# Kernel optimization log

Hardware: AMD Instinct MI355X
Metric: run time of the kernel (lower is better)

The kernel has to match this reference:

```python
import jax, jax.numpy as jnp
import numpy as np

WINDOW = (4, 8, 8)  # (T, Wh, Ww)
NUM_HEADS = 4


def _rel_position_index(ws):
    T, Wh, Ww = ws
    coords = np.stack(np.meshgrid(np.arange(T), np.arange(Wh), np.arange(Ww), indexing='ij'))
    cf = coords.reshape(3, -1)  # [3, N]
    rc = (cf[:, :, None] - cf[:, None, :]).transpose(1, 2, 0).astype(np.int64)  # [N, N, 3]
    rc[..., 0] += T - 1
    rc[..., 1] += Wh - 1
    rc[..., 2] += Ww - 1
    rc[..., 0] *= (2 * Wh - 1) * (2 * Ww - 1)
    rc[..., 1] *= (2 * Ww - 1)
    return rc.sum(-1).astype(np.int32)  # [N, N]


def setup_inputs() -> dict:
    key = jax.random.key(0)
    ks = jax.random.split(key, 5)
    B_, C = 1024, 128
    N = WINDOW[0] * WINDOW[1] * WINDOW[2]
    table_len = (2 * WINDOW[0] - 1) * (2 * WINDOW[1] - 1) * (2 * WINDOW[2] - 1)
    return {
        'x': jax.random.normal(ks[0], (B_, N, C), dtype=jnp.float32),
        'q_w': jax.random.normal(ks[1], (C, C), dtype=jnp.float32) * 0.02,
        'kv_w': jax.random.normal(ks[2], (C, 2 * C), dtype=jnp.float32) * 0.02,
        'proj_w': jax.random.normal(ks[3], (C, C), dtype=jnp.float32) * 0.02,
        'proj_b': jnp.zeros((C,), dtype=jnp.float32),
        'rpb_table': jax.random.normal(ks[4], (table_len, NUM_HEADS), dtype=jnp.float32) * 0.02,
        'rel_index': jnp.asarray(_rel_position_index(WINDOW)),
    }


def reference(x, q_w, kv_w, proj_w, proj_b, rpb_table, rel_index):
    B, N, C = x.shape
    H = NUM_HEADS
    Dh = C // H
    T = WINDOW[0]
    interval = WINDOW[1] * WINDOW[2]
    scale = Dh ** -0.5
    # qkv projections (no bias, eval-mode: dropout is identity)
    q = (x @ q_w).reshape(B, N, H, Dh).transpose(0, 2, 1, 3)      # [B,H,N,Dh]
    kv = (x @ kv_w).reshape(B, N, 2, H, Dh)
    k = kv[:, :, 0].transpose(0, 2, 1, 3)                          # [B,H,N,Dh]
    v = kv[:, :, 1].transpose(0, 2, 1, 3)
    all_ids = np.arange(N)
    outs = []
    for i in range(T):  # fixed small loop over time slices
        qb, qe = i * interval, (i + 1) * interval
        other = np.concatenate([all_ids[:qb], all_ids[qe:]])      # keys = all other frames
        q_i = q[:, :, qb:qe]                                      # [B,H,Nq,Dh]
        k_o = k[:, :, other]                                      # [B,H,Nk,Dh]
        v_o = v[:, :, other]
        # gathered relative position bias: [Nq,Nk,H] -> [1,H,Nq,Nk]
        bias = rpb_table[rel_index[qb:qe][:, other]]
        attn = jnp.einsum('bhqd,bhkd->bhqk', q_i * scale, k_o) + bias.transpose(2, 0, 1)[None]
        attn = jax.nn.softmax(attn, axis=-1)
        out = jnp.einsum('bhqk,bhkd->bhqd', attn, v_o)            # [B,H,Nq,Dh]
        outs.append(out.transpose(0, 2, 1, 3).reshape(B, interval, C))
    x_out = jnp.concatenate(outs, axis=1)                         # [B,N,C]
    return x_out @ proj_w + proj_b
```

## Files before the change

kernel.cpp:

```cpp
#include <hip/hip_runtime.h>
#include <hip/hip_bf16.h>


typedef float  f32x16 __attribute__((ext_vector_type(16)));
typedef float  f32x4_ __attribute__((ext_vector_type(4)));
typedef __bf16 bf16x8 __attribute__((ext_vector_type(8)));
typedef __bf16 bf16x2 __attribute__((ext_vector_type(2)));
typedef unsigned int  uint32x4_ __attribute__((ext_vector_type(4)));
typedef unsigned int  uint32x2_ __attribute__((ext_vector_type(2)));

#define MFMA32(a, b, c) __builtin_amdgcn_mfma_f32_32x32x16_bf16((a), (b), (c), 0, 0, 0)

static __device__ __forceinline__ unsigned int packbf2(float a, float b) {
  bf16x2 t = { (__bf16)a, (__bf16)b };
  return __builtin_bit_cast(unsigned int, t);
}
static __device__ __forceinline__ void plswap(unsigned int &a, unsigned int &b) {
  asm volatile("v_permlane32_swap_b32 %0, %1" : "+v"(a), "+v"(b));
}

#define XS_OFF 0
#define QL_OFF 65536
#define KL_OFF 81920
#define VT_OFF 98304
#define OH_OFF 114688

static __device__ __forceinline__ int swzA(int row, int off) {
  return (row << 6) + (off ^ (((row >> 1) & 3) << 4));
}
static __device__ __forceinline__ int swzX(int row, int off) {
  return (row << 8) + (off ^ ((row & 7) << 4));
}
static __device__ __forceinline__ int swzV(int row, int off) {
  return (row << 9) + (off ^ ((row & 7) << 4));
}

__global__ void prep_kernel(const float* __restrict__ qw, const float* __restrict__ kvw,
                            const float* __restrict__ pw, const float* __restrict__ rpb,
                            const int* __restrict__ relidx,
                            float* __restrict__ biasT, unsigned short* __restrict__ qwt,
                            unsigned short* __restrict__ kwt, unsigned short* __restrict__ vwt,
                            unsigned short* __restrict__ pwt) {
  int gid = blockIdx.x * 256 + threadIdx.x;
  if (gid < 262144) {
    int key = gid & 255;
    int ql  = (gid >> 8) & 63;
    int h   = (gid >> 14) & 3;
    int i   = gid >> 16;
    float v;
    if ((key >> 6) == i) v = -1.0e30f;
    else                 v = rpb[relidx[(i * 64 + ql) * 256 + key] * 4 + h];
    biasT[gid] = v;
  } else {
    int wid = gid - 262144;
    if (wid < 16384) {
      int cin = wid & 127, cout = wid >> 7;
      qwt[wid] = __builtin_bit_cast(unsigned short, (__bf16)(qw[cin * 128 + cout] * 0.17677669529663687f));
      kwt[wid] = __builtin_bit_cast(unsigned short, (__bf16)(kvw[cin * 256 + cout]));
      vwt[wid] = __builtin_bit_cast(unsigned short, (__bf16)(kvw[cin * 256 + 128 + cout]));
      pwt[wid] = __builtin_bit_cast(unsigned short, (__bf16)(pw[cin * 128 + cout]));
    }
  }
}

__global__ __launch_bounds__(512, 2) void fused_attn(
    const float* __restrict__ x, const float* __restrict__ biasT,
    const unsigned short* __restrict__ qwt, const unsigned short* __restrict__ kwt,
    const unsigned short* __restrict__ vwt, const unsigned short* __restrict__ pwt,
    const float* __restrict__ proj_b, float* __restrict__ out) {
  __shared__ __align__(16) char smem[131072];
  const int tid  = threadIdx.x;
  const int w    = tid >> 6;
  const int lane = tid & 63;
  const int lq   = lane & 31;
  const int lh   = lane >> 5;
  const int b    = blockIdx.x;

  const float* xb = x + (size_t)b * (256 * 128);
  #pragma unroll
  for (int it = 0; it < 16; ++it) {
    int idx = it * 512 + tid;
    f32x4_ v = ((const f32x4_*)xb)[idx];
    int n = idx >> 5, c4 = idx & 31;
    uint32x2_ wv = { packbf2(v[0], v[1]), packbf2(v[2], v[3]) };
    *(uint32x2_*)(smem + XS_OFF + swzX(n, c4 * 8)) = wv;
  }
  __syncthreads();

  f32x16 yacc[4];
  #pragma unroll
  for (int nt = 0; nt < 4; ++nt)
    #pragma unroll
    for (int r = 0; r < 16; ++r) yacc[nt][r] = 0.0f;

  for (int h = 0; h < 4; ++h) {
    f32x16 qa, ka, va;
    #pragma unroll
    for (int r = 0; r < 16; ++r) { qa[r] = 0.0f; ka[r] = 0.0f; va[r] = 0.0f; }
    const int wrow = h * 32 + lq;
    #pragma unroll
    for (int ks = 0; ks < 8; ++ks) {
      bf16x8 xf = *(const bf16x8*)(smem + XS_OFF + swzX(w * 32 + lq, ks * 32 + lh * 16));
      bf16x8 wq = *(const bf16x8*)(qwt + wrow * 128 + ks * 16 + lh * 8);
      bf16x8 wk = *(const bf16x8*)(kwt + wrow * 128 + ks * 16 + lh * 8);
      bf16x8 wv = *(const bf16x8*)(vwt + wrow * 128 + ks * 16 + lh * 8);
      qa = MFMA32(wq, xf, qa);
      ka = MFMA32(wk, xf, ka);
      va = MFMA32(xf, wv, va);
    }
    #pragma unroll
    for (int g = 0; g < 4; ++g) {
      uint32x2_ q2 = { packbf2(qa[4*g+0], qa[4*g+1]), packbf2(qa[4*g+2], qa[4*g+3]) };
      *(uint32x2_*)(smem + QL_OFF + swzA(w * 32 + lq, g * 16 + lh * 8)) = q2;
      uint32x2_ k2 = { packbf2(ka[4*g+0], ka[4*g+1]), packbf2(ka[4*g+2], ka[4*g+3]) };
      *(uint32x2_*)(smem + KL_OFF + swzA(w * 32 + lq, g * 16 + lh * 8)) = k2;
      uint32x2_ v2 = { packbf2(va[4*g+0], va[4*g+1]), packbf2(va[4*g+2], va[4*g+3]) };
      *(uint32x2_*)(smem + VT_OFF + swzV(lq, w * 64 + g * 16 + lh * 8)) = v2;
    }
    __syncthreads();

    const int iblk   = w >> 1;
    const int qlocal = (w & 1) * 32 + lq;
    const float* biasW = biasT + (((iblk * 4 + h) * 64 + qlocal) * 256);
    bf16x8 qb0 = *(const bf16x8*)(smem + QL_OFF + swzA(w * 32 + lq, lh * 16));
    bf16x8 qb1 = *(const bf16x8*)(smem + QL_OFF + swzA(w * 32 + lq, 32 + lh * 16));

    f32x16 S[8];
    #pragma unroll
    for (int kt = 0; kt < 8; ++kt) {
      f32x16 c;
      #pragma unroll
      for (int g = 0; g < 4; ++g) {
        f32x4_ bv = *(const f32x4_*)(biasW + kt * 32 + lh * 4 + g * 8);
        c[4*g+0] = bv[0]; c[4*g+1] = bv[1]; c[4*g+2] = bv[2]; c[4*g+3] = bv[3];
      }
      bf16x8 ka0 = *(const bf16x8*)(smem + KL_OFF + swzA(kt * 32 + lq, lh * 16));
      bf16x8 ka1 = *(const bf16x8*)(smem + KL_OFF + swzA(kt * 32 + lq, 32 + lh * 16));
      c = MFMA32(ka0, qb0, c);
      c = MFMA32(ka1, qb1, c);
      S[kt] = c;
    }
    float m = -3.0e38f;
    #pragma unroll
    for (int kt = 0; kt < 8; ++kt)
      #pragma unroll
      for (int r = 0; r < 16; ++r) m = fmaxf(m, S[kt][r]);
    m = fmaxf(m, __shfl_xor(m, 32, 64));
    float l = 0.0f;
    #pragma unroll
    for (int kt = 0; kt < 8; ++kt)
      #pragma unroll
      for (int r = 0; r < 16; ++r) { float e = __expf(S[kt][r] - m); S[kt][r] = e; l += e; }
    l += __shfl_xor(l, 32, 64);
    float linv = 1.0f / l;

    f32x16 pv;
    #pragma unroll
    for (int r = 0; r < 16; ++r) pv[r] = 0.0f;
    #pragma unroll
    for (int kt = 0; kt < 8; ++kt) {
      unsigned int pk0 = packbf2(S[kt][0],  S[kt][1]);
      unsigned int pk1 = packbf2(S[kt][2],  S[kt][3]);
      unsigned int pk2 = packbf2(S[kt][4],  S[kt][5]);
      unsigned int pk3 = packbf2(S[kt][6],  S[kt][7]);
      unsigned int pk4 = packbf2(S[kt][8],  S[kt][9]);
      unsigned int pk5 = packbf2(S[kt][10], S[kt][11]);
      unsigned int pk6 = packbf2(S[kt][12], S[kt][13]);
      unsigned int pk7 = packbf2(S[kt][14], S[kt][15]);
      plswap(pk0, pk2); plswap(pk1, pk3);
      plswap(pk4, pk6); plswap(pk5, pk7);
      uint32x4_ f0 = { pk0, pk1, pk2, pk3 };
      uint32x4_ f1 = { pk4, pk5, pk6, pk7 };
      bf16x8 b0 = __builtin_bit_cast(bf16x8, f0);
      bf16x8 b1 = __builtin_bit_cast(bf16x8, f1);
      bf16x8 va0 = *(const bf16x8*)(smem + VT_OFF + swzV(lq, kt * 64 + lh * 16));
      bf16x8 va1 = *(const bf16x8*)(smem + VT_OFF + swzV(lq, kt * 64 + 32 + lh * 16));
      pv = MFMA32(va0, b0, pv);
      pv = MFMA32(va1, b1, pv);
    }
    #pragma unroll
    for (int g = 0; g < 4; ++g) {
      uint32x2_ o2 = { packbf2(pv[4*g+0] * linv, pv[4*g+1] * linv),
                       packbf2(pv[4*g+2] * linv, pv[4*g+3] * linv) };
      *(uint32x2_*)(smem + OH_OFF + swzA(w * 32 + lq, g * 16 + lh * 8)) = o2;
    }
    __syncthreads();

    bf16x8 a0 = *(const bf16x8*)(smem + OH_OFF + swzA(w * 32 + lq, lh * 16));
    bf16x8 a1 = *(const bf16x8*)(smem + OH_OFF + swzA(w * 32 + lq, 32 + lh * 16));
    #pragma unroll
    for (int nt = 0; nt < 4; ++nt) {
      bf16x8 pb0 = *(const bf16x8*)(pwt + (nt * 32 + lq) * 128 + h * 32 + lh * 8);
      bf16x8 pb1 = *(const bf16x8*)(pwt + (nt * 32 + lq) * 128 + h * 32 + 16 + lh * 8);
      yacc[nt] = MFMA32(a0, pb0, yacc[nt]);
      yacc[nt] = MFMA32(a1, pb1, yacc[nt]);
    }
  }

  float* yb = out + (size_t)b * (256 * 128);
  #pragma unroll
  for (int nt = 0; nt < 4; ++nt) {
    float pbv = proj_b[nt * 32 + lq];
    #pragma unroll
    for (int g = 0; g < 4; ++g)
      #pragma unroll
      for (int r2 = 0; r2 < 4; ++r2) {
        int n = w * 32 + 8 * g + 4 * lh + r2;
        yb[n * 128 + nt * 32 + lq] = yacc[nt][4 * g + r2] + pbv;
      }
  }
}

extern "C" void kernel_launch(void* const* d_in, const int* in_sizes, int n_in,
                              void* d_out, int out_size, void* d_ws, size_t ws_size,
                              hipStream_t stream) {
  (void)in_sizes; (void)n_in; (void)out_size; (void)ws_size;
  const float* x      = (const float*)d_in[0];
  const float* qw     = (const float*)d_in[1];
  const float* kvw    = (const float*)d_in[2];
  const float* pw     = (const float*)d_in[3];
  const float* pb     = (const float*)d_in[4];
  const float* rpb    = (const float*)d_in[5];
  const int*   relidx = (const int*)d_in[6];
  float* out = (float*)d_out;

  char* ws = (char*)d_ws;
  float* biasT          = (float*)ws;
  unsigned short* qwt   = (unsigned short*)(ws + 1048576);
  unsigned short* kwt   = (unsigned short*)(ws + 1048576 + 32768);
  unsigned short* vwt   = (unsigned short*)(ws + 1048576 + 65536);
  unsigned short* pwt   = (unsigned short*)(ws + 1048576 + 98304);

  prep_kernel<<<dim3(1088), dim3(256), 0, stream>>>(qw, kvw, pw, rpb, relidx,
                                                    biasT, qwt, kwt, vwt, pwt);
  fused_attn<<<dim3(1024), dim3(512), 0, stream>>>(x, biasT, qwt, kwt, vwt, pwt, pb, out);
}
```

Before: 519.1 us.

## Software-pipeline next-head QKV projection with PV matmul using double-buffered K/V

The per-head loop now computes the next head's Q/K/V projection MFMAs interleaved with the current head's PV MFMAs, writing K/V into double-buffered LDS slots so one barrier per head suffices. Q is kept in registers via permlane swaps instead of going through LDS. The x fragments are hoisted into registers, and the output projection is deferred to a single pass after all heads by writing per-head outputs over the x tile. Softmax max and sum reductions are also restructured into trees. This raises register pressure, which risks spills or lower occupancy.

After: 551.5 us. 6.2% more time.

```diff
diff --git a/kernel.cpp b/kernel.cpp
--- a/kernel.cpp
+++ b/kernel.cpp
@@ -19,11 +19,26 @@
   asm volatile("v_permlane32_swap_b32 %0, %1" : "+v"(a), "+v"(b));
 }
 
-#define XS_OFF 0
-#define QL_OFF 65536
-#define KL_OFF 81920
-#define VT_OFF 98304
-#define OH_OFF 114688
+static __device__ __forceinline__ float max16(const f32x16& v) {
+  float a0 = fmaxf(v[0], v[1]),  a1 = fmaxf(v[2], v[3]);
+  float a2 = fmaxf(v[4], v[5]),  a3 = fmaxf(v[6], v[7]);
+  float a4 = fmaxf(v[8], v[9]),  a5 = fmaxf(v[10], v[11]);
+  float a6 = fmaxf(v[12], v[13]), a7 = fmaxf(v[14], v[15]);
+  float b0 = fmaxf(a0, a1), b1 = fmaxf(a2, a3), b2 = fmaxf(a4, a5), b3 = fmaxf(a6, a7);
+  return fmaxf(fmaxf(b0, b1), fmaxf(b2, b3));
+}
+static __device__ __forceinline__ float sum16(const f32x16& v) {
+  float a0 = v[0] + v[1],  a1 = v[2] + v[3],  a2 = v[4] + v[5],  a3 = v[6] + v[7];
+  float a4 = v[8] + v[9],  a5 = v[10] + v[11], a6 = v[12] + v[13], a7 = v[14] + v[15];
+  float b0 = a0 + a1, b1 = a2 + a3, b2 = a4 + a5, b3 = a6 + a7;
+  return (b0 + b1) + (b2 + b3);
+}
+
+#define K0_OFF 0
+#define V0_OFF 16384
+#define K1_OFF 32768
+#define V1_OFF 49152
+#define XS_OFF 65536
 
 static __device__ __forceinline__ int swzA(int row, int off) {
   return (row << 6) + (off ^ (((row >> 1) & 3) << 4));
@@ -87,45 +102,55 @@
   }
   __syncthreads();
 
-  f32x16 yacc[4];
-  #pragma unroll
-  for (int nt = 0; nt < 4; ++nt)
-    #pragma unroll
-    for (int r = 0; r < 16; ++r) yacc[nt][r] = 0.0f;
-
+  bf16x8 xf[8];
+  #pragma unroll
+  for (int ks = 0; ks < 8; ++ks)
+    xf[ks] = *(const bf16x8*)(smem + XS_OFF + swzX(w * 32 + lq, ks * 32 + lh * 16));
+
+  bf16x8 qb0, qb1;
+  {
+    f32x16 gq, gk, gv;
+    #pragma unroll
+    for (int r = 0; r < 16; ++r) { gq[r] = 0.0f; gk[r] = 0.0f; gv[r] = 0.0f; }
+    #pragma unroll
+    for (int ks = 0; ks < 8; ++ks) {
+      bf16x8 wq = *(const bf16x8*)(qwt + lq * 128 + ks * 16 + lh * 8);
+      bf16x8 wk = *(const bf16x8*)(kwt + lq * 128 + ks * 16 + lh * 8);
+      bf16x8 wv = *(const bf16x8*)(vwt + lq * 128 + ks * 16 + lh * 8);
+      gq = MFMA32(wq, xf[ks], gq);
+      gk = MFMA32(wk, xf[ks], gk);
+      gv = MFMA32(xf[ks], wv, gv);
+    }
+    unsigned int u0 = packbf2(gq[0], gq[1]),  u2 = packbf2(gq[4], gq[5]);
+    unsigned int u1 = packbf2(gq[2], gq[3]),  u3 = packbf2(gq[6], gq[7]);
+    plswap(u0, u2); plswap(u1, u3);
+    uint32x4_ f0 = { u0, u1, u2, u3 };
+    qb0 = __builtin_bit_cast(bf16x8, f0);
+    unsigned int v0 = packbf2(gq[8], gq[9]),   v2 = packbf2(gq[12], gq[13]);
+    unsigned int v1 = packbf2(gq[10], gq[11]), v3 = packbf2(gq[14], gq[15]);
+    plswap(v0, v2); plswap(v1, v3);
+    uint32x4_ f1 = { v0, v1, v2, v3 };
+    qb1 = __builtin_bit_cast(bf16x8, f1);
+    #pragma unroll
+    for (int g = 0; g < 4; ++g) {
+      uint32x2_ k2 = { packbf2(gk[4*g+0], gk[4*g+1]), packbf2(gk[4*g+2], gk[4*g+3]) };
+      *(uint32x2_*)(smem + K0_OFF + swzA(w * 32 + lq, g * 16 + lh * 8)) = k2;
+      uint32x2_ v2_ = { packbf2(gv[4*g+0], gv[4*g+1]), packbf2(gv[4*g+2], gv[4*g+3]) };
+      *(uint32x2_*)(smem + V0_OFF + swzV(lq, w * 64 + g * 16 + lh * 8)) = v2_;
+    }
+  }
+  __syncthreads();
+
+  #pragma unroll
   for (int h = 0; h < 4; ++h) {
-    f32x16 qa, ka, va;
-    #pragma unroll
-    for (int r = 0; r < 16; ++r) { qa[r] = 0.0f; ka[r] = 0.0f; va[r] = 0.0f; }
-    const int wrow = h * 32 + lq;
-    #pragma unroll
-    for (int ks = 0; ks < 8; ++ks) {
-      bf16x8 xf = *(const bf16x8*)(smem + XS_OFF + swzX(w * 32 + lq, ks * 32 + lh * 16));
-      bf16x8 wq = *(const bf16x8*)(qwt + wrow * 128 + ks * 16 + lh * 8);
-      bf16x8 wk = *(const bf16x8*)(kwt + wrow * 128 + ks * 16 + lh * 8);
-      bf16x8 wv = *(const bf16x8*)(vwt + wrow * 128 + ks * 16 + lh * 8);
-      qa = MFMA32(wq, xf, qa);
-      ka = MFMA32(wk, xf, ka);
-      va = MFMA32(xf, wv, va);
-    }
-    #pragma unroll
-    for (int g = 0; g < 4; ++g) {
-      uint32x2_ q2 = { packbf2(qa[4*g+0], qa[4*g+1]), packbf2(qa[4*g+2], qa[4*g+3]) };
-      *(uint32x2_*)(smem + QL_OFF + swzA(w * 32 + lq, g * 16 + lh * 8)) = q2;
-      uint32x2_ k2 = { packbf2(ka[4*g+0], ka[4*g+1]), packbf2(ka[4*g+2], ka[4*g+3]) };
-      *(uint32x2_*)(smem + KL_OFF + swzA(w * 32 + lq, g * 16 + lh * 8)) = k2;
-      uint32x2_ v2 = { packbf2(va[4*g+0], va[4*g+1]), packbf2(va[4*g+2], va[4*g+3]) };
-      *(uint32x2_*)(smem + VT_OFF + swzV(lq, w * 64 + g * 16 + lh * 8)) = v2;
-    }
-    __syncthreads();
-
-    const int iblk   = w >> 1;
-    const int qlocal = (w & 1) * 32 + lq;
-    const float* biasW = biasT + (((iblk * 4 + h) * 64 + qlocal) * 256);
-    bf16x8 qb0 = *(const bf16x8*)(smem + QL_OFF + swzA(w * 32 + lq, lh * 16));
-    bf16x8 qb1 = *(const bf16x8*)(smem + QL_OFF + swzA(w * 32 + lq, 32 + lh * 16));
+    const int KB = (h & 1) ? K1_OFF : K0_OFF;
+    const int VB = (h & 1) ? V1_OFF : V0_OFF;
+    const int KN = (h & 1) ? K0_OFF : K1_OFF;
+    const int VN = (h & 1) ? V0_OFF : V1_OFF;
+    const float* biasW = biasT + ((((w >> 1) * 4 + h) * 64 + (w & 1) * 32 + lq) * 256);
 
     f32x16 S[8];
+    float pm[8];
     #pragma unroll
     for (int kt = 0; kt < 8; ++kt) {
       f32x16 c;
@@ -134,29 +159,31 @@
         f32x4_ bv = *(const f32x4_*)(biasW + kt * 32 + lh * 4 + g * 8);
         c[4*g+0] = bv[0]; c[4*g+1] = bv[1]; c[4*g+2] = bv[2]; c[4*g+3] = bv[3];
       }
-      bf16x8 ka0 = *(const bf16x8*)(smem + KL_OFF + swzA(kt * 32 + lq, lh * 16));
-      bf16x8 ka1 = *(const bf16x8*)(smem + KL_OFF + swzA(kt * 32 + lq, 32 + lh * 16));
+      bf16x8 ka0 = *(const bf16x8*)(smem + KB + swzA(kt * 32 + lq, lh * 16));
+      bf16x8 ka1 = *(const bf16x8*)(smem + KB + swzA(kt * 32 + lq, 32 + lh * 16));
       c = MFMA32(ka0, qb0, c);
       c = MFMA32(ka1, qb1, c);
       S[kt] = c;
-    }
-    float m = -3.0e38f;
-    #pragma unroll
-    for (int kt = 0; kt < 8; ++kt)
-      #pragma unroll
-      for (int r = 0; r < 16; ++r) m = fmaxf(m, S[kt][r]);
+      pm[kt] = max16(c);
+    }
+    float m = fmaxf(fmaxf(fmaxf(pm[0], pm[1]), fmaxf(pm[2], pm[3])),
+                    fmaxf(fmaxf(pm[4], pm[5]), fmaxf(pm[6], pm[7])));
     m = fmaxf(m, __shfl_xor(m, 32, 64));
-    float l = 0.0f;
-    #pragma unroll
-    for (int kt = 0; kt < 8; ++kt)
-      #pragma unroll
-      for (int r = 0; r < 16; ++r) { float e = __expf(S[kt][r] - m); S[kt][r] = e; l += e; }
+    float ps[8];
+    #pragma unroll
+    for (int kt = 0; kt < 8; ++kt) {
+      #pragma unroll
+      for (int r = 0; r < 16; ++r) S[kt][r] = __expf(S[kt][r] - m);
+      ps[kt] = sum16(S[kt]);
+    }
+    float l = ((ps[0] + ps[1]) + (ps[2] + ps[3])) + ((ps[4] + ps[5]) + (ps[6] + ps[7]));
     l += __shfl_xor(l, 32, 64);
     float linv = 1.0f / l;
 
-    f32x16 pv;
-    #pragma unroll
-    for (int r = 0; r < 16; ++r) pv[r] = 0.0f;
+    f32x16 pv, gq, gk, gv;
+    #pragma unroll
+    for (int r = 0; r < 16; ++r) { pv[r] = 0.0f; gq[r] = 0.0f; gk[r] = 0.0f; gv[r] = 0.0f; }
+    const int wrow = (h + 1) * 32 + lq;
     #pragma unroll
     for (int kt = 0; kt < 8; ++kt) {
       unsigned int pk0 = packbf2(S[kt][0],  S[kt][1]);
@@ -171,29 +198,63 @@
       plswap(pk4, pk6); plswap(pk5, pk7);
       uint32x4_ f0 = { pk0, pk1, pk2, pk3 };
       uint32x4_ f1 = { pk4, pk5, pk6, pk7 };
-      bf16x8 b0 = __builtin_bit_cast(bf16x8, f0);
-      bf16x8 b1 = __builtin_bit_cast(bf16x8, f1);
-      bf16x8 va0 = *(const bf16x8*)(smem + VT_OFF + swzV(lq, kt * 64 + lh * 16));
-      bf16x8 va1 = *(const bf16x8*)(smem + VT_OFF + swzV(lq, kt * 64 + 32 + lh * 16));
-      pv = MFMA32(va0, b0, pv);
-      pv = MFMA32(va1, b1, pv);
-    }
+      bf16x8 pb0 = __builtin_bit_cast(bf16x8, f0);
+      bf16x8 pb1 = __builtin_bit_cast(bf16x8, f1);
+      bf16x8 vl0 = *(const bf16x8*)(smem + VB + swzV(lq, kt * 64 + lh * 16));
+      bf16x8 vl1 = *(const bf16x8*)(smem + VB + swzV(lq, kt * 64 + 32 + lh * 16));
+      pv = MFMA32(vl0, pb0, pv);
+      pv = MFMA32(vl1, pb1, pv);
+      if (h < 3) {
+        bf16x8 wq = *(const bf16x8*)(qwt + wrow * 128 + kt * 16 + lh * 8);
+        bf16x8 wk = *(const bf16x8*)(kwt + wrow * 128 + kt * 16 + lh * 8);
+        bf16x8 wv = *(const bf16x8*)(vwt + wrow * 128 + kt * 16 + lh * 8);
+        gq = MFMA32(wq, xf[kt], gq);
+        gk = MFMA32(wk, xf[kt], gk);
+        gv = MFMA32(xf[kt], wv, gv);
+      }
+    }
+
     #pragma unroll
     for (int g = 0; g < 4; ++g) {
       uint32x2_ o2 = { packbf2(pv[4*g+0] * linv, pv[4*g+1] * linv),
                        packbf2(pv[4*g+2] * linv, pv[4*g+3] * linv) };
-      *(uint32x2_*)(smem + OH_OFF + swzA(w * 32 + lq, g * 16 + lh * 8)) = o2;
-    }
-    __syncthreads();
-
-    bf16x8 a0 = *(const bf16x8*)(smem + OH_OFF + swzA(w * 32 + lq, lh * 16));
-    bf16x8 a1 = *(const bf16x8*)(smem + OH_OFF + swzA(w * 32 + lq, 32 + lh * 16));
+      *(uint32x2_*)(smem + XS_OFF + swzX(w * 32 + lq, h * 64 + g * 16 + lh * 8)) = o2;
+    }
+
+    if (h < 3) {
+      unsigned int u0 = packbf2(gq[0], gq[1]),  u2 = packbf2(gq[4], gq[5]);
+      unsigned int u1 = packbf2(gq[2], gq[3]),  u3 = packbf2(gq[6], gq[7]);
+      plswap(u0, u2); plswap(u1, u3);
+      uint32x4_ f0 = { u0, u1, u2, u3 };
+      qb0 = __builtin_bit_cast(bf16x8, f0);
+      unsigned int v0 = packbf2(gq[8], gq[9]),   v2 = packbf2(gq[12], gq[13]);
+      unsigned int v1 = packbf2(gq[10], gq[11]), v3 = packbf2(gq[14], gq[15]);
+      plswap(v0, v2); plswap(v1, v3);
+      uint32x4_ f1 = { v0, v1, v2, v3 };
+      qb1 = __builtin_bit_cast(bf16x8, f1);
+      #pragma unroll
+      for (int g = 0; g < 4; ++g) {
+        uint32x2_ k2 = { packbf2(gk[4*g+0], gk[4*g+1]), packbf2(gk[4*g+2], gk[4*g+3]) };
+        *(uint32x2_*)(smem + KN + swzA(w * 32 + lq, g * 16 + lh * 8)) = k2;
+        uint32x2_ v2_ = { packbf2(gv[4*g+0], gv[4*g+1]), packbf2(gv[4*g+2], gv[4*g+3]) };
+        *(uint32x2_*)(smem + VN + swzV(lq, w * 64 + g * 16 + lh * 8)) = v2_;
+      }
+      __syncthreads();
+    }
+  }
+
+  f32x16 yacc[4];
+  #pragma unroll
+  for (int nt = 0; nt < 4; ++nt)
+    #pragma unroll
+    for (int r = 0; r < 16; ++r) yacc[nt][r] = 0.0f;
+  #pragma unroll
+  for (int s = 0; s < 8; ++s) {
+    bf16x8 as = *(const bf16x8*)(smem + XS_OFF + swzX(w * 32 + lq, s * 32 + lh * 16));
     #pragma unroll
     for (int nt = 0; nt < 4; ++nt) {
-      bf16x8 pb0 = *(const bf16x8*)(pwt + (nt * 32 + lq) * 128 + h * 32 + lh * 8);
-      bf16x8 pb1 = *(const bf16x8*)(pwt + (nt * 32 + lq) * 128 + h * 32 + 16 + lh * 8);
-      yacc[nt] = MFMA32(a0, pb0, yacc[nt]);
-      yacc[nt] = MFMA32(a1, pb1, yacc[nt]);
+      bf16x8 pb = *(const bf16x8*)(pwt + (nt * 32 + lq) * 128 + s * 16 + lh * 8);
+      yacc[nt] = MFMA32(as, pb, yacc[nt]);
     }
   }
 
```
